# Kernel tuning notes

Hardware: AMD Instinct MI355X
Metric: run time of the kernel (lower is better)

The kernel has to match this reference:

```python
import jax, jax.numpy as jnp
import numpy as np

B, S, E, U = 4, 512, 512, 256

def setup_inputs() -> dict:
    key = jax.random.key(0)
    k1, k2, k3, k4 = jax.random.split(key, 4)
    h1 = jax.random.normal(k1, (B, S, E), dtype=jnp.float32)
    h2 = jax.random.normal(k2, (B, S, E), dtype=jnp.float32)
    # glorot-ish scaled weights
    w = jax.random.normal(k3, (2 * E, U), dtype=jnp.float32) * (2.0 / (2 * E + U)) ** 0.5
    b1 = jnp.zeros((U,), dtype=jnp.float32)
    v = jax.random.normal(k4, (U, 1), dtype=jnp.float32) * (2.0 / (U + 1)) ** 0.5
    b2 = jnp.zeros((1,), dtype=jnp.float32)
    return {"h1": h1, "h2": h2, "w": w, "b1": b1, "v": v, "b2": b2}

def reference(h1, h2, w, b1, v, b2):
    # Original: for each query step i, concat([h1, repeat(h2[:,i])]) @ w.
    # Split w so the concat-matmul becomes two separate projections:
    #   concat([h1_j, h2_i]) @ w == h1_j @ w1 + h2_i @ w2
    E_ = h1.shape[-1]
    w1, w2 = w[:E_], w[E_:]
    key_pre = jnp.einsum('bje,eu->bju', h1, w1)   # [B,Sk,U]
    qry_pre = jnp.einsum('bie,eu->biu', h2, w2)   # [B,Sq,U]
    # energy: [B,Sq,Sk,U]
    t = jnp.tanh(qry_pre[:, :, None, :] + key_pre[:, None, :, :] + b1)
    scores = jnp.einsum('biju,uo->bij', t, v) + b2[0]  # [B,Sq,Sk]
    p = jax.nn.softmax(scores, axis=-1)                # softmax over keys j
    # context per query: sum_j p[b,i,j] * h1[b,j]
    return jnp.einsum('bij,bje->bie', p, h1)           # [B,S,E]
```

## Files before the change

kernel.cpp:

```cpp
#include <hip/hip_runtime.h>
#include <hip/hip_bf16.h>

#define B_ 4
#define S_ 512
#define E_ 512
#define U_ 256

#define KC 2.885390081777927f

#if __has_builtin(__builtin_amdgcn_exp2f)
#define EXP2F(x) __builtin_amdgcn_exp2f(x)
#else
#define EXP2F(x) __exp2f(x)
#endif
#if __has_builtin(__builtin_amdgcn_rcpf)
#define RCPF(x) __builtin_amdgcn_rcpf(x)
#else
#define RCPF(x) (1.0f / (x))
#endif

typedef __attribute__((ext_vector_type(8))) short bf16x8;
typedef __attribute__((ext_vector_type(4))) float f32x4;

__device__ __forceinline__ unsigned short bf16rn(float x) {
    unsigned int u = __float_as_uint(x);
    u = (u + 0x7FFFu + ((u >> 16) & 1u)) >> 16;
    return (unsigned short)u;
}
__device__ __forceinline__ void splitT(float x, short* hi, short* lo) {
    const unsigned u = __float_as_uint(x);
    *hi = (short)(u >> 16);
    const float hf = __uint_as_float(u & 0xFFFF0000u);
    *lo = (short)(__float_as_uint(x - hf) >> 16);
}

__global__ __launch_bounds__(256) void prep_gemm(
    const float* __restrict__ h1, const float* __restrict__ h2,
    const float* __restrict__ w, const float* __restrict__ b1,
    float* __restrict__ keySt, float* __restrict__ qryS,
    bf16x8* __restrict__ h1c)
{
    __shared__ unsigned short WhiL[16][64][8];
    __shared__ unsigned short WloL[16][64][8];

    const int tid = threadIdx.x;
    const int bid = blockIdx.x;

    if (bid < 1024) {
        const int z = bid >> 9, ng = (bid >> 5) & 15, mq = bid & 31;

        const int l16c = tid & 15, r16 = tid >> 4;
        const float* __restrict__ Wp = w + (size_t)z * E_ * U_ + ng * 16 + l16c;
#pragma unroll 4
        for (int it = 0; it < 32; ++it) {
            const int k = it * 16 + r16;
            short h, l;
            splitT(Wp[(size_t)k * U_] * KC, &h, &l);
            const int kc = k >> 5, quad = (k >> 3) & 3, jj = k & 7;
            WhiL[kc][quad * 16 + l16c][jj] = (unsigned short)h;
            WloL[kc][quad * 16 + l16c][jj] = (unsigned short)l;
        }
        __syncthreads();

        const int wv = tid >> 6, lane = tid & 63;
        const int quad = lane >> 4, l16 = lane & 15;
        const int m0 = (mq * 4 + wv) * 16;
        const float* __restrict__ Arow = (z ? h2 : h1) + (size_t)(m0 + l16) * E_;

        f32x4 acc = (f32x4){0.f, 0.f, 0.f, 0.f};

        for (int kc = 0; kc < 16; ++kc) {
            const int kb = kc * 32 + quad * 8;
            const float4 x0 = *(const float4*)&Arow[kb];
            const float4 x1 = *(const float4*)&Arow[kb + 4];
            const float xs[8] = {x0.x, x0.y, x0.z, x0.w, x1.x, x1.y, x1.z, x1.w};
            bf16x8 ah, al;
#pragma unroll
            for (int j = 0; j < 8; ++j) {
                short h, l; splitT(xs[j], &h, &l);
                ah[j] = h; al[j] = l;
            }
            const bf16x8 bh = *(const bf16x8*)&WhiL[kc][lane][0];
            const bf16x8 bl = *(const bf16x8*)&WloL[kc][lane][0];
            acc = __builtin_amdgcn_mfma_f32_16x16x32_bf16(ah, bh, acc, 0, 0, 0);
            acc = __builtin_amdgcn_mfma_f32_16x16x32_bf16(ah, bl, acc, 0, 0, 0);
            acc = __builtin_amdgcn_mfma_f32_16x16x32_bf16(al, bh, acc, 0, 0, 0);
        }

        const int u = ng * 16 + l16;
        if (z == 0) {
            const int b = m0 >> 9;
            const int j0 = (m0 & (S_ - 1)) + quad * 4;
            *(float4*)&keySt[((size_t)b * U_ + u) * S_ + j0] =
                make_float4(acc[0], acc[1], acc[2], acc[3]);
        } else {
            const int row = m0 + quad * 4;
            const float bias = KC * b1[u];
#pragma unroll
            for (int r = 0; r < 4; ++r)
                qryS[(size_t)(row + r) * U_ + u] = acc[r] + bias;
        }
    } else {
        const int s = (bid - 1024) * 256 + tid;
        const int lane = s & 63, kc = (s >> 6) & 15, et = (s >> 10) & 31, b = s >> 15;
        const int quad = lane >> 4, l16 = lane & 15;
        const float* __restrict__ src =
            h1 + ((size_t)b * S_ + kc * 32 + quad * 8) * E_ + et * 16 + l16;
        bf16x8 c;
#pragma unroll
        for (int j = 0; j < 8; ++j)
            c[j] = (short)bf16rn(src[(size_t)j * E_]);
        h1c[s] = c;
    }
}

__device__ __forceinline__ float quadTerm(float a0, float a1, float a2, float a3,
                                          float4 vq, float acc) {
    const float F1 = EXP2F(a0) + 1.f;
    const float F2 = EXP2F(a1) + 1.f;
    const float F3 = EXP2F(a2) + 1.f;
    const float F4 = EXP2F(a3) + 1.f;
    const float P12 = F1 * F2, P34 = F3 * F4;
    const float n12 = fmaf(vq.y, F1, vq.x * F2);
    const float n34 = fmaf(vq.w, F3, vq.z * F4);
    const float num = fmaf(n34, P12, n12 * P34);
    return fmaf(num, RCPF(P12 * P34), acc);
}

__global__ __launch_bounds__(512) void scores_kernel(
    const float* __restrict__ keySt, const float* __restrict__ qryS,
    const float* __restrict__ v, unsigned short* __restrict__ Pp)
{
    const int i0 = blockIdx.x * 4;
    const int b = blockIdx.y;
    const int t = threadIdx.x;
    const int wv = t >> 6;

    __shared__ float ssm[8][4];

    const float4* __restrict__ q0v = (const float4*)(qryS + ((size_t)b * S_ + i0) * U_);
    const float4* __restrict__ q1v = q0v + (U_ / 4);
    const float4* __restrict__ q2v = q0v + 2 * (U_ / 4);
    const float4* __restrict__ q3v = q0v + 3 * (U_ / 4);
    const float4* __restrict__ vv4 = (const float4*)v;
    const float* __restrict__ kp = keySt + (size_t)b * U_ * S_ + t;

    float a0 = 0.f, a1 = 0.f, a2 = 0.f, a3 = 0.f;
    float k0 = kp[0], k1 = kp[S_], k2 = kp[2 * S_], k3 = kp[3 * S_];
    kp += 4 * S_;
#pragma unroll 4
    for (int ub = 0; ub < U_ / 4 - 1; ++ub) {
        const float n0 = kp[0], n1 = kp[S_], n2 = kp[2 * S_], n3 = kp[3 * S_];
        kp += 4 * S_;
        const float4 vq = vv4[ub];
        const float4 q0 = q0v[ub], q1 = q1v[ub], q2 = q2v[ub], q3 = q3v[ub];
        a0 = quadTerm(q0.x + k0, q0.y + k1, q0.z + k2, q0.w + k3, vq, a0);
        a1 = quadTerm(q1.x + k0, q1.y + k1, q1.z + k2, q1.w + k3, vq, a1);
        a2 = quadTerm(q2.x + k0, q2.y + k1, q2.z + k2, q2.w + k3, vq, a2);
        a3 = quadTerm(q3.x + k0, q3.y + k1, q3.z + k2, q3.w + k3, vq, a3);
        k0 = n0; k1 = n1; k2 = n2; k3 = n3;
    }
    {
        const int ub = U_ / 4 - 1;
        const float4 vq = vv4[ub];
        const float4 q0 = q0v[ub], q1 = q1v[ub], q2 = q2v[ub], q3 = q3v[ub];
        a0 = quadTerm(q0.x + k0, q0.y + k1, q0.z + k2, q0.w + k3, vq, a0);
        a1 = quadTerm(q1.x + k0, q1.y + k1, q1.z + k2, q1.w + k3, vq, a1);
        a2 = quadTerm(q2.x + k0, q2.y + k1, q2.z + k2, q2.w + k3, vq, a2);
        a3 = quadTerm(q3.x + k0, q3.y + k1, q3.z + k2, q3.w + k3, vq, a3);
    }

    const float p0 = EXP2F(-a0 * KC);
    const float p1 = EXP2F(-a1 * KC);
    const float p2 = EXP2F(-a2 * KC);
    const float p3 = EXP2F(-a3 * KC);
    float s0 = p0, s1 = p1, s2 = p2, s3 = p3;
#pragma unroll
    for (int off = 1; off < 64; off <<= 1) {
        s0 += __shfl_xor(s0, off, 64);
        s1 += __shfl_xor(s1, off, 64);
        s2 += __shfl_xor(s2, off, 64);
        s3 += __shfl_xor(s3, off, 64);
    }
    if ((t & 63) == 0) {
        ssm[wv][0] = s0; ssm[wv][1] = s1; ssm[wv][2] = s2; ssm[wv][3] = s3;
    }
    __syncthreads();
    s0 = ssm[0][0]; s1 = ssm[0][1]; s2 = ssm[0][2]; s3 = ssm[0][3];
#pragma unroll
    for (int k = 1; k < 8; ++k) {
        s0 += ssm[k][0]; s1 += ssm[k][1]; s2 += ssm[k][2]; s3 += ssm[k][3];
    }
    const float r0 = RCPF(s0), r1 = RCPF(s1), r2 = RCPF(s2), r3 = RCPF(s3);

    const int itile = i0 >> 4;
    const int base = (itile * 16 + (t >> 5)) * 64 + (((t >> 3) & 3) << 4);
    unsigned short* __restrict__ pb = Pp + (size_t)b * S_ * S_;
    const int io = i0 & 15, jo = t & 7;
    pb[((base + io + 0) << 3) + jo] = bf16rn(p0 * r0);
    pb[((base + io + 1) << 3) + jo] = bf16rn(p1 * r1);
    pb[((base + io + 2) << 3) + jo] = bf16rn(p2 * r2);
    pb[((base + io + 3) << 3) + jo] = bf16rn(p3 * r3);
}

__global__ __launch_bounds__(256) void pv_gemm(
    const unsigned short* __restrict__ Pp, const bf16x8* __restrict__ h1c,
    float* __restrict__ out)
{
    const int tid = threadIdx.x;
    const int wv = tid >> 6, lane = tid & 63;
    const int quad = lane >> 4, l16 = lane & 15;
    const int wt = blockIdx.x * 4 + wv;
    const int b = wt >> 10, rem = wt & 1023;
    const int it = rem >> 5, et = rem & 31;

    const bf16x8* __restrict__ Ab =
        (const bf16x8*)(Pp + (size_t)b * S_ * S_) + (it * 16) * 64 + lane;
    const bf16x8* __restrict__ Bb =
        h1c + ((b * 32 + et) * 16) * 64 + lane;

    f32x4 acc = (f32x4){0.f, 0.f, 0.f, 0.f};

    for (int kc = 0; kc < 16; ++kc) {
        const bf16x8 a8 = Ab[kc * 64];
        const bf16x8 b8 = Bb[kc * 64];
        acc = __builtin_amdgcn_mfma_f32_16x16x32_bf16(a8, b8, acc, 0, 0, 0);
    }

    const int i = it * 16 + quad * 4;
    const int e = et * 16 + l16;
    float* __restrict__ ob = out + ((size_t)b * S_ + i) * E_ + e;
#pragma unroll
    for (int r = 0; r < 4; ++r)
        ob[(size_t)r * E_] = acc[r];
}

extern "C" void kernel_launch(void* const* d_in, const int* in_sizes, int n_in,
                              void* d_out, int out_size, void* d_ws, size_t ws_size,
                              hipStream_t stream) {
    const float* h1 = (const float*)d_in[0];
    const float* h2 = (const float*)d_in[1];
    const float* w  = (const float*)d_in[2];
    const float* b1 = (const float*)d_in[3];
    const float* v  = (const float*)d_in[4];
    float* out = (float*)d_out;

    char* ws = (char*)d_ws;
    float* keySt = (float*)ws;                 ws += 2u << 20;
    float* qryS  = (float*)ws;                 ws += 2u << 20;
    unsigned short* Pp = (unsigned short*)ws;  ws += 2u << 20;
    bf16x8* h1c = (bf16x8*)ws;

    prep_gemm<<<dim3(1536), dim3(256), 0, stream>>>(h1, h2, w, b1, keySt, qryS, h1c);
    scores_kernel<<<dim3(S_ / 4, B_), dim3(512), 0, stream>>>(keySt, qryS, v, Pp);
    pv_gemm<<<dim3(1024), dim3(256), 0, stream>>>(Pp, h1c, out);
}
```

Baseline: 139.2 us.

## Fuse score softmax and PV MFMA into one kernel via LDS staging

Merges the scores kernel and the PV GEMM into one kernel. Each block now computes 8 query rows of normalized probabilities, stages them as bf16 in LDS (zero-padding the other half of a 16-row MFMA tile), and then runs the 16x16x32 bf16 MFMA against h1c directly. This removes the global round-trip of the probability matrix and one kernel launch. The cost is wasted MFMA work on padded rows, every block re-reading all of h1c for its batch, and a grid half the previous size.

Measured after the change: 145.6 us. 1.05x slower.

```diff
diff --git a/kernel.cpp b/kernel.cpp
--- a/kernel.cpp
+++ b/kernel.cpp
@@ -127,112 +127,98 @@
     return fmaf(num, RCPF(P12 * P34), acc);
 }
 
-__global__ __launch_bounds__(512) void scores_kernel(
+#define PLD 520
+
+__global__ __launch_bounds__(512) void scores_pv(
     const float* __restrict__ keySt, const float* __restrict__ qryS,
-    const float* __restrict__ v, unsigned short* __restrict__ Pp)
+    const float* __restrict__ v, const bf16x8* __restrict__ h1c,
+    float* __restrict__ out)
 {
-    const int i0 = blockIdx.x * 4;
+    const int i0 = blockIdx.x * 8;
     const int b = blockIdx.y;
     const int t = threadIdx.x;
     const int wv = t >> 6;
 
-    __shared__ float ssm[8][4];
-
-    const float4* __restrict__ q0v = (const float4*)(qryS + ((size_t)b * S_ + i0) * U_);
-    const float4* __restrict__ q1v = q0v + (U_ / 4);
-    const float4* __restrict__ q2v = q0v + 2 * (U_ / 4);
-    const float4* __restrict__ q3v = q0v + 3 * (U_ / 4);
+    __shared__ unsigned short Pl[16][PLD];
+    __shared__ float ssm[8][8];
+
+    const float4* __restrict__ qv =
+        (const float4*)(qryS + ((size_t)b * S_ + i0) * U_);
     const float4* __restrict__ vv4 = (const float4*)v;
     const float* __restrict__ kp = keySt + (size_t)b * U_ * S_ + t;
 
-    float a0 = 0.f, a1 = 0.f, a2 = 0.f, a3 = 0.f;
-    float k0 = kp[0], k1 = kp[S_], k2 = kp[2 * S_], k3 = kp[3 * S_];
-    kp += 4 * S_;
-#pragma unroll 4
-    for (int ub = 0; ub < U_ / 4 - 1; ++ub) {
-        const float n0 = kp[0], n1 = kp[S_], n2 = kp[2 * S_], n3 = kp[3 * S_];
-        kp += 4 * S_;
+    float a[8];
+#pragma unroll
+    for (int r = 0; r < 8; ++r) a[r] = 0.f;
+
+#pragma unroll 2
+    for (int ub = 0; ub < U_ / 4; ++ub) {
+        const float k0 = kp[(size_t)(ub * 4 + 0) * S_];
+        const float k1 = kp[(size_t)(ub * 4 + 1) * S_];
+        const float k2 = kp[(size_t)(ub * 4 + 2) * S_];
+        const float k3 = kp[(size_t)(ub * 4 + 3) * S_];
         const float4 vq = vv4[ub];
-        const float4 q0 = q0v[ub], q1 = q1v[ub], q2 = q2v[ub], q3 = q3v[ub];
-        a0 = quadTerm(q0.x + k0, q0.y + k1, q0.z + k2, q0.w + k3, vq, a0);
-        a1 = quadTerm(q1.x + k0, q1.y + k1, q1.z + k2, q1.w + k3, vq, a1);
-        a2 = quadTerm(q2.x + k0, q2.y + k1, q2.z + k2, q2.w + k3, vq, a2);
-        a3 = quadTerm(q3.x + k0, q3.y + k1, q3.z + k2, q3.w + k3, vq, a3);
-        k0 = n0; k1 = n1; k2 = n2; k3 = n3;
-    }
-    {
-        const int ub = U_ / 4 - 1;
-        const float4 vq = vv4[ub];
-        const float4 q0 = q0v[ub], q1 = q1v[ub], q2 = q2v[ub], q3 = q3v[ub];
-        a0 = quadTerm(q0.x + k0, q0.y + k1, q0.z + k2, q0.w + k3, vq, a0);
-        a1 = quadTerm(q1.x + k0, q1.y + k1, q1.z + k2, q1.w + k3, vq, a1);
-        a2 = quadTerm(q2.x + k0, q2.y + k1, q2.z + k2, q2.w + k3, vq, a2);
-        a3 = quadTerm(q3.x + k0, q3.y + k1, q3.z + k2, q3.w + k3, vq, a3);
-    }
-
-    const float p0 = EXP2F(-a0 * KC);
-    const float p1 = EXP2F(-a1 * KC);
-    const float p2 = EXP2F(-a2 * KC);
-    const float p3 = EXP2F(-a3 * KC);
-    float s0 = p0, s1 = p1, s2 = p2, s3 = p3;
-#pragma unroll
-    for (int off = 1; off < 64; off <<= 1) {
-        s0 += __shfl_xor(s0, off, 64);
-        s1 += __shfl_xor(s1, off, 64);
-        s2 += __shfl_xor(s2, off, 64);
-        s3 += __shfl_xor(s3, off, 64);
-    }
-    if ((t & 63) == 0) {
-        ssm[wv][0] = s0; ssm[wv][1] = s1; ssm[wv][2] = s2; ssm[wv][3] = s3;
-    }
+#pragma unroll
+        for (int r = 0; r < 8; ++r) {
+            const float4 q = qv[r * 64 + ub];
+            a[r] = quadTerm(q.x + k0, q.y + k1, q.z + k2, q.w + k3, vq, a[r]);
+        }
+    }
+
+    float p[8], s[8];
+#pragma unroll
+    for (int r = 0; r < 8; ++r) {
+        p[r] = EXP2F(-a[r] * KC);
+        s[r] = p[r];
+    }
+#pragma unroll
+    for (int off = 1; off < 64; off <<= 1)
+#pragma unroll
+        for (int r = 0; r < 8; ++r) s[r] += __shfl_xor(s[r], off, 64);
+    if ((t & 63) == 0)
+#pragma unroll
+        for (int r = 0; r < 8; ++r) ssm[wv][r] = s[r];
     __syncthreads();
-    s0 = ssm[0][0]; s1 = ssm[0][1]; s2 = ssm[0][2]; s3 = ssm[0][3];
-#pragma unroll
-    for (int k = 1; k < 8; ++k) {
-        s0 += ssm[k][0]; s1 += ssm[k][1]; s2 += ssm[k][2]; s3 += ssm[k][3];
-    }
-    const float r0 = RCPF(s0), r1 = RCPF(s1), r2 = RCPF(s2), r3 = RCPF(s3);
-
+#pragma unroll
+    for (int r = 0; r < 8; ++r) {
+        float acc = ssm[0][r];
+#pragma unroll
+        for (int k = 1; k < 8; ++k) acc += ssm[k][r];
+        s[r] = RCPF(acc);
+    }
+
+    const int io = i0 & 15;
+#pragma unroll
+    for (int r = 0; r < 8; ++r) {
+        Pl[io + r][t] = bf16rn(p[r] * s[r]);
+        Pl[(io ^ 8) + r][t] = 0;
+    }
+    __syncthreads();
+
+    const int lane = t & 63;
+    const int quad = lane >> 4, l16 = lane & 15;
     const int itile = i0 >> 4;
-    const int base = (itile * 16 + (t >> 5)) * 64 + (((t >> 3) & 3) << 4);
-    unsigned short* __restrict__ pb = Pp + (size_t)b * S_ * S_;
-    const int io = i0 & 15, jo = t & 7;
-    pb[((base + io + 0) << 3) + jo] = bf16rn(p0 * r0);
-    pb[((base + io + 1) << 3) + jo] = bf16rn(p1 * r1);
-    pb[((base + io + 2) << 3) + jo] = bf16rn(p2 * r2);
-    pb[((base + io + 3) << 3) + jo] = bf16rn(p3 * r3);
-}
-
-__global__ __launch_bounds__(256) void pv_gemm(
-    const unsigned short* __restrict__ Pp, const bf16x8* __restrict__ h1c,
-    float* __restrict__ out)
-{
-    const int tid = threadIdx.x;
-    const int wv = tid >> 6, lane = tid & 63;
-    const int quad = lane >> 4, l16 = lane & 15;
-    const int wt = blockIdx.x * 4 + wv;
-    const int b = wt >> 10, rem = wt & 1023;
-    const int it = rem >> 5, et = rem & 31;
-
-    const bf16x8* __restrict__ Ab =
-        (const bf16x8*)(Pp + (size_t)b * S_ * S_) + (it * 16) * 64 + lane;
-    const bf16x8* __restrict__ Bb =
-        h1c + ((b * 32 + et) * 16) * 64 + lane;
-
-    f32x4 acc = (f32x4){0.f, 0.f, 0.f, 0.f};
-
-    for (int kc = 0; kc < 16; ++kc) {
-        const bf16x8 a8 = Ab[kc * 64];
-        const bf16x8 b8 = Bb[kc * 64];
-        acc = __builtin_amdgcn_mfma_f32_16x16x32_bf16(a8, b8, acc, 0, 0, 0);
-    }
-
-    const int i = it * 16 + quad * 4;
-    const int e = et * 16 + l16;
-    float* __restrict__ ob = out + ((size_t)b * S_ + i) * E_ + e;
-#pragma unroll
-    for (int r = 0; r < 4; ++r)
-        ob[(size_t)r * E_] = acc[r];
+    const int row16 = quad * 4;
+    const bool live = (row16 & 8) == io;
+
+#pragma unroll
+    for (int e = 0; e < 4; ++e) {
+        const int et = wv * 4 + e;
+        const bf16x8* __restrict__ Bb = h1c + ((b * 32 + et) * 16) * 64 + lane;
+        f32x4 acc = (f32x4){0.f, 0.f, 0.f, 0.f};
+#pragma unroll
+        for (int kc = 0; kc < 16; ++kc) {
+            const bf16x8 a8 = *(const bf16x8*)&Pl[l16][kc * 32 + quad * 8];
+            acc = __builtin_amdgcn_mfma_f32_16x16x32_bf16(a8, Bb[kc * 64], acc, 0, 0, 0);
+        }
+        if (live) {
+            const int ig = itile * 16 + row16;
+            float* __restrict__ ob = out + ((size_t)b * S_ + ig) * E_ + et * 16 + l16;
+#pragma unroll
+            for (int r = 0; r < 4; ++r)
+                ob[(size_t)r * E_] = acc[r];
+        }
+    }
 }
 
 extern "C" void kernel_launch(void* const* d_in, const int* in_sizes, int n_in,
@@ -246,12 +232,10 @@
     float* out = (float*)d_out;
 
     char* ws = (char*)d_ws;
-    float* keySt = (float*)ws;                 ws += 2u << 20;
-    float* qryS  = (float*)ws;                 ws += 2u << 20;
-    unsigned short* Pp = (unsigned short*)ws;  ws += 2u << 20;
+    float* keySt = (float*)ws;   ws += 2u << 20;
+    float* qryS  = (float*)ws;   ws += 2u << 20;
     bf16x8* h1c = (bf16x8*)ws;
 
     prep_gemm<<<dim3(1536), dim3(256), 0, stream>>>(h1, h2, w, b1, keySt, qryS, h1c);
-    scores_kernel<<<dim3(S_ / 4, B_), dim3(512), 0, stream>>>(keySt, qryS, v, Pp);
-    pv_gemm<<<dim3(1024), dim3(256), 0, stream>>>(Pp, h1c, out);
-}
+    scores_pv<<<dim3(S_ / 8, B_), dim3(512), 0, stream>>>(keySt, qryS, v, h1c, out);
+}
```
